# Kernel optimization log

Measured on AMD Instinct MI355X. Metric: run time of the kernel, lower is better.

The kernel has to match this reference:

```python
import jax, jax.numpy as jnp
import numpy as np

E_ROUTER = 32      # routed experts with real FFNs
ZERO_E = 8         # zero-experts (identity skip)
TOP_K = 4
ROUTED_SCALE = 2.5


def setup_inputs() -> dict:
    key = jax.random.key(0)
    k1, k2, k3, k4, k5 = jax.random.split(key, 5)
    T, H, I = 2048, 1024, 512
    N = E_ROUTER + ZERO_E
    return {
        "hidden_states": jax.random.normal(k1, (T, H), jnp.float32),
        "router_w": jax.random.normal(k2, (N, H), jnp.float32) * 0.02,            # classifier weight [N, H]
        "e_score_correction_bias": jax.random.normal(k3, (N,), jnp.float32) * 0.01,
        "w13": jax.random.normal(k4, (E_ROUTER, 2 * I, H), jnp.float32) * 0.02,   # gate+up per expert
        "w2": jax.random.normal(k5, (E_ROUTER, H, I), jnp.float32) * 0.02,        # down proj per expert
    }


def reference(hidden_states, router_w, e_score_correction_bias, w13, w2):
    T, H = hidden_states.shape
    I = w2.shape[-1]

    # --- router (LongcatFlashTopkRouter) ---
    logits = hidden_states @ router_w.T                         # [T, N]
    scores = jax.nn.softmax(logits, axis=-1)
    biased = scores + e_score_correction_bias[None, :]
    _, topk_ids = jax.lax.top_k(biased, TOP_K)                  # indices chosen on biased scores
    topk_w = jnp.take_along_axis(scores, topk_ids, axis=-1) * ROUTED_SCALE  # weights from unbiased scores

    # --- zero experts: ids >= E_ROUTER contribute weight * x directly ---
    zero_mask = topk_ids >= E_ROUTER
    zero_total = jnp.sum(jnp.where(zero_mask, topk_w, 0.0), axis=-1, keepdims=True)  # [T,1]
    zero_expert_output = hidden_states * zero_total
    topk_w = jnp.where(zero_mask, 0.0, topk_w)
    topk_ids = jnp.where(zero_mask, 0, topk_ids)

    # --- combine weights per (token, expert): scatter-add of topk weights ---
    combine = jnp.zeros((T, E_ROUTER), jnp.float32).at[
        jnp.arange(T)[:, None], topk_ids
    ].add(topk_w)                                               # [T, E]

    # --- experts: swiglu FFN per expert (dense form of grouped GEMM; zero combine
    #     weights make it mathematically identical to dispatch/compute/combine) ---
    gate_up = jnp.einsum('th,eih->eti', hidden_states, w13)     # [E, T, 2I]
    gate, up = gate_up[..., :I], gate_up[..., I:]
    h = jax.nn.silu(gate) * up                                  # [E, T, I]
    expert_out = jnp.einsum('eti,ehi->eth', h, w2)              # [E, T, H]
    routed = jnp.einsum('eth,te->th', expert_out, combine)      # [T, H]

    return routed + zero_expert_output
```

## Files before the change

kernel.cpp:

```cpp
#include <hip/hip_runtime.h>
#include <math.h>

#define TT 2048
#define HH 1024
#define NE 40
#define ER 32
#define II 512
#define TOPK 4
#define RSCALE 2.5f
#define MAXW 64

typedef __bf16 bf16x8 __attribute__((ext_vector_type(8)));
typedef float f32x4 __attribute__((ext_vector_type(4)));

__global__ __launch_bounds__(256) void k_router(const float* __restrict__ hidden,
                                                const float* __restrict__ rw,
                                                const float* __restrict__ bias,
                                                float* __restrict__ out,
                                                int* __restrict__ tok4_id,
                                                float* __restrict__ tok4_w,
                                                __bf16* __restrict__ hid_bf) {
  int lane = threadIdx.x & 63;
  int t = blockIdx.x * 4 + (threadIdx.x >> 6);
  const float* hrow = hidden + (size_t)t * HH;
  float4 hv[4];
  #pragma unroll
  for (int c = 0; c < 4; c++) hv[c] = *(const float4*)(hrow + c * 256 + lane * 4);

  float mylg = -INFINITY;
  for (int e = 0; e < NE; e++) {
    const float* wrow = rw + (size_t)e * HH;
    float p = 0.f;
    #pragma unroll
    for (int c = 0; c < 4; c++) {
      float4 w4 = *(const float4*)(wrow + c * 256 + lane * 4);
      p += hv[c].x * w4.x + hv[c].y * w4.y + hv[c].z * w4.z + hv[c].w * w4.w;
    }
    #pragma unroll
    for (int off = 32; off; off >>= 1) p += __shfl_xor(p, off);
    if (lane == e) mylg = p;
  }
  float m = mylg;
  #pragma unroll
  for (int off = 32; off; off >>= 1) m = fmaxf(m, __shfl_xor(m, off));
  float p = (lane < NE) ? expf(mylg - m) : 0.f;
  float s = p;
  #pragma unroll
  for (int off = 32; off; off >>= 1) s += __shfl_xor(s, off);
  float score = p / s;
  float v = (lane < NE) ? score + bias[lane] : -INFINITY;
  int ids[TOPK]; float wv[TOPK];
  #pragma unroll
  for (int k = 0; k < TOPK; k++) {
    float mv = v;
    int mi = (lane < NE) ? lane : 63;
    #pragma unroll
    for (int off = 32; off; off >>= 1) {
      float ov = __shfl_xor(mv, off);
      int oi = __shfl_xor(mi, off);
      if (ov > mv || (ov == mv && oi < mi)) { mv = ov; mi = oi; }
    }
    ids[k] = mi;
    wv[k] = RSCALE * __shfl(score, mi);
    if (lane == mi) v = -INFINITY;
  }
  float zt = 0.f;
  #pragma unroll
  for (int k = 0; k < TOPK; k++) if (ids[k] >= ER) zt += wv[k];
  if (lane == 0) {
    #pragma unroll
    for (int k = 0; k < TOPK; k++) {
      tok4_id[t * TOPK + k] = ids[k];
      tok4_w[t * TOPK + k] = wv[k];
    }
  }
  #pragma unroll
  for (int c = 0; c < 4; c++) {
    int j = c * 256 + lane * 4;
    float4 h4 = hv[c];
    *(float4*)(out + (size_t)t * HH + j) =
        make_float4(h4.x * zt, h4.y * zt, h4.z * zt, h4.w * zt);
    union { __bf16 h[4]; uint2 u; } pk;
    pk.h[0] = (__bf16)h4.x; pk.h[1] = (__bf16)h4.y;
    pk.h[2] = (__bf16)h4.z; pk.h[3] = (__bf16)h4.w;
    *(uint2*)(hid_bf + (size_t)t * HH + j) = pk.u;
  }
}

__global__ __launch_bounds__(256) void k_scanscatter(const int* __restrict__ tok4_id,
                                                     const float* __restrict__ tok4_w,
                                                     int* __restrict__ cnt,
                                                     int* __restrict__ offs,
                                                     int* __restrict__ wl_e,
                                                     int* __restrict__ wl_m0,
                                                     int* __restrict__ nwork,
                                                     int* __restrict__ pair_tok,
                                                     float* __restrict__ pair_w) {
  __shared__ int scnt[32];
  __shared__ int scur[32];
  int tid = threadIdx.x;
  if (tid < 32) scnt[tid] = 0;
  __syncthreads();
  int ids[32]; float wv[32];
  #pragma unroll
  for (int i = 0; i < 32; i++) {
    int idx = i * 256 + tid;
    ids[i] = tok4_id[idx];
    wv[i] = tok4_w[idx];
    if (ids[i] < ER) atomicAdd(&scnt[ids[i]], 1);
  }
  __syncthreads();
  if (tid < 64) {
    int lane = tid;
    int c = (lane < ER) ? scnt[lane] : 0;
    int ts = (c + 255) >> 8;
    int ps = c, pt = ts;
    #pragma unroll
    for (int off = 1; off < 32; off <<= 1) {
      int v1 = __shfl_up(ps, off);
      int v2 = __shfl_up(pt, off);
      if (lane >= off) { ps += v1; pt += v2; }
    }
    if (lane < ER) {
      int o = ps - c;
      offs[lane] = o; cnt[lane] = c; scur[lane] = o;
      int tb = pt - ts;
      for (int i = 0; i < ts; i++) { wl_e[tb + i] = lane; wl_m0[tb + i] = i * 256; }
    }
    if (lane == 31) *nwork = pt;
  }
  __syncthreads();
  #pragma unroll
  for (int i = 0; i < 32; i++) {
    if (ids[i] < ER) {
      int pos = atomicAdd(&scur[ids[i]], 1);
      pair_tok[pos] = (i * 256 + tid) >> 2;
      pair_w[pos] = wv[i];
    }
  }
}

__global__ __launch_bounds__(256) void k_w13(const __bf16* __restrict__ hid_bf,
                                             const float* __restrict__ w13,
                                             const int* __restrict__ cnt,
                                             const int* __restrict__ offs,
                                             const int* __restrict__ pair_tok,
                                             const int* __restrict__ wl_e,
                                             const int* __restrict__ wl_m0,
                                             const int* __restrict__ nwork,
                                             __bf16* __restrict__ h_buf) {
  int bx = blockIdx.x;
  if (bx >= *nwork) return;
  int e = wl_e[bx], m0w = wl_m0[bx];
  int M = cnt[e] - m0w; if (M > 256) M = 256;
  int base = offs[e] + m0w;
  int n0 = blockIdx.y * 32;

  __shared__ __bf16 As[256][72];
  __shared__ __bf16 Bs[64][72];
  __shared__ int tl[256];

  int tid = threadIdx.x;
  int lane = tid & 63, w = tid >> 6;
  int quad = lane >> 4, rr = lane & 15;

  tl[tid] = pair_tok[base + ((tid < M) ? tid : 0)];

  const float* wg_base = w13 + (size_t)e * (2 * II) * HH + (size_t)n0 * HH;
  const float* wu_base = w13 + (size_t)e * (2 * II) * HH + (size_t)(II + n0) * HH;

  f32x4 accg[4][2] = {};
  f32x4 accu[4][2] = {};
  __syncthreads();

  for (int k0 = 0; k0 < HH; k0 += 64) {
    #pragma unroll
    for (int p = 0; p < 8; p++) {
      int s = p * 256 + tid;
      int r = s >> 3, c = (s & 7) * 8;
      *(uint4*)&As[r][c] = *(const uint4*)(hid_bf + (size_t)tl[r] * HH + k0 + c);
    }
    #pragma unroll
    for (int p = 0; p < 4; p++) {
      int s = p * 256 + tid;
      int r = s >> 4, c = (s & 15) * 4;
      const float* src = ((r < 32) ? (wg_base + (size_t)r * HH)
                                   : (wu_base + (size_t)(r - 32) * HH)) + k0 + c;
      float4 v = *(const float4*)src;
      union { __bf16 h[4]; uint2 u; } pk;
      pk.h[0] = (__bf16)v.x; pk.h[1] = (__bf16)v.y;
      pk.h[2] = (__bf16)v.z; pk.h[3] = (__bf16)v.w;
      *(uint2*)&Bs[r][c] = pk.u;
    }
    __syncthreads();
    #pragma unroll
    for (int ks = 0; ks < 2; ks++) {
      int kb = ks * 32 + quad * 8;
      bf16x8 a[4], bg[2], bu[2];
      #pragma unroll
      for (int i = 0; i < 4; i++) a[i] = *(const bf16x8*)&As[w * 64 + i * 16 + rr][kb];
      #pragma unroll
      for (int j = 0; j < 2; j++) {
        bg[j] = *(const bf16x8*)&Bs[j * 16 + rr][kb];
        bu[j] = *(const bf16x8*)&Bs[32 + j * 16 + rr][kb];
      }
      #pragma unroll
      for (int i = 0; i < 4; i++)
        #pragma unroll
        for (int j = 0; j < 2; j++) {
          accg[i][j] = __builtin_amdgcn_mfma_f32_16x16x32_bf16(a[i], bg[j], accg[i][j], 0, 0, 0);
          accu[i][j] = __builtin_amdgcn_mfma_f32_16x16x32_bf16(a[i], bu[j], accu[i][j], 0, 0, 0);
        }
    }
    __syncthreads();
  }
  #pragma unroll
  for (int i = 0; i < 4; i++)
    #pragma unroll
    for (int j = 0; j < 2; j++)
      #pragma unroll
      for (int l = 0; l < 4; l++) {
        int m = w * 64 + i * 16 + quad * 4 + l;
        if (m < M) {
          float g = accg[i][j][l], u = accu[i][j][l];
          float hv = g / (1.f + expf(-g)) * u;
          h_buf[(size_t)(base + m) * II + n0 + j * 16 + rr] = (__bf16)hv;
        }
      }
}

__global__ __launch_bounds__(256) void k_w2(const __bf16* __restrict__ h_buf,
                                            const float* __restrict__ w2,
                                            const int* __restrict__ cnt,
                                            const int* __restrict__ offs,
                                            const int* __restrict__ pair_tok,
                                            const float* __restrict__ pair_w,
                                            const int* __restrict__ wl_e,
                                            const int* __restrict__ wl_m0,
                                            const int* __restrict__ nwork,
                                            float* __restrict__ out) {
  int bx = blockIdx.x;
  if (bx >= *nwork) return;
  int e = wl_e[bx], m0w = wl_m0[bx];
  int M = cnt[e] - m0w; if (M > 256) M = 256;
  int base = offs[e] + m0w;
  int h0 = blockIdx.y * 64;

  __shared__ __bf16 As[256][72];
  __shared__ __bf16 Bs[64][72];
  __shared__ int tl[256];
  __shared__ float wl[256];

  int tid = threadIdx.x;
  int lane = tid & 63, w = tid >> 6;
  int quad = lane >> 4, rr = lane & 15;

  {
    int ok = tid < M;
    tl[tid] = ok ? pair_tok[base + tid] : 0;
    wl[tid] = ok ? pair_w[base + tid] : 0.f;
  }
  const __bf16* h_base = h_buf + (size_t)base * II;
  const float* w_base = w2 + (size_t)e * HH * II + (size_t)h0 * II;

  f32x4 acc[4][4] = {};
  __syncthreads();

  for (int k0 = 0; k0 < II; k0 += 64) {
    #pragma unroll
    for (int p = 0; p < 8; p++) {
      int s = p * 256 + tid;
      int r = s >> 3, c = (s & 7) * 8;
      *(uint4*)&As[r][c] = *(const uint4*)(h_base + (size_t)r * II + k0 + c);
    }
    #pragma unroll
    for (int p = 0; p < 4; p++) {
      int s = p * 256 + tid;
      int r = s >> 4, c = (s & 15) * 4;
      float4 v = *(const float4*)(w_base + (size_t)r * II + k0 + c);
      union { __bf16 h[4]; uint2 u; } pk;
      pk.h[0] = (__bf16)v.x; pk.h[1] = (__bf16)v.y;
      pk.h[2] = (__bf16)v.z; pk.h[3] = (__bf16)v.w;
      *(uint2*)&Bs[r][c] = pk.u;
    }
    __syncthreads();
    #pragma unroll
    for (int ks = 0; ks < 2; ks++) {
      int kb = ks * 32 + quad * 8;
      bf16x8 a[4], b[4];
      #pragma unroll
      for (int i = 0; i < 4; i++) a[i] = *(const bf16x8*)&As[w * 64 + i * 16 + rr][kb];
      #pragma unroll
      for (int j = 0; j < 4; j++) b[j] = *(const bf16x8*)&Bs[j * 16 + rr][kb];
      #pragma unroll
      for (int i = 0; i < 4; i++)
        #pragma unroll
        for (int j = 0; j < 4; j++)
          acc[i][j] = __builtin_amdgcn_mfma_f32_16x16x32_bf16(a[i], b[j], acc[i][j], 0, 0, 0);
    }
    __syncthreads();
  }
  #pragma unroll
  for (int i = 0; i < 4; i++)
    #pragma unroll
    for (int l = 0; l < 4; l++) {
      int m = w * 64 + i * 16 + quad * 4 + l;
      if (m < M) {
        int t = tl[m];
        float wp = wl[m];
        #pragma unroll
        for (int j = 0; j < 4; j++)
          atomicAdd(&out[(size_t)t * HH + h0 + j * 16 + rr], acc[i][j][l] * wp);
      }
    }
}

extern "C" void kernel_launch(void* const* d_in, const int* in_sizes, int n_in,
                              void* d_out, int out_size, void* d_ws, size_t ws_size,
                              hipStream_t stream) {
  const float* hidden = (const float*)d_in[0];
  const float* rw     = (const float*)d_in[1];
  const float* bias   = (const float*)d_in[2];
  const float* w13    = (const float*)d_in[3];
  const float* w2     = (const float*)d_in[4];
  float* out = (float*)d_out;

  int* ws_i = (int*)d_ws;
  int* tok4_id = ws_i;
  float* tok4_w = (float*)(tok4_id + TT * TOPK);
  int* pair_tok = (int*)(tok4_w + TT * TOPK);
  float* pair_w = (float*)(pair_tok + TT * TOPK);
  int* cnt = (int*)(pair_w + TT * TOPK);
  int* offs = cnt + 32;
  int* wl_e = offs + 32;
  int* wl_m0 = wl_e + 64;
  int* nwork = wl_m0 + 64;
  __bf16* hid_bf = (__bf16*)(nwork + 64);
  __bf16* h_buf = hid_bf + (size_t)TT * HH;

  k_router<<<dim3(TT / 4), dim3(256), 0, stream>>>(hidden, rw, bias, out,
                                                   tok4_id, tok4_w, hid_bf);
  k_scanscatter<<<dim3(1), dim3(256), 0, stream>>>(tok4_id, tok4_w, cnt, offs,
                                                   wl_e, wl_m0, nwork, pair_tok, pair_w);
  k_w13<<<dim3(MAXW, 16), dim3(256), 0, stream>>>(hid_bf, w13, cnt, offs, pair_tok,
                                                  wl_e, wl_m0, nwork, h_buf);
  k_w2<<<dim3(MAXW, 16), dim3(256), 0, stream>>>(h_buf, w2, cnt, offs, pair_tok, pair_w,
                                                 wl_e, wl_m0, nwork, out);
}
```

Baseline: 340.8 us.

## Double-buffer expert GEMMs with async LDS loads, swizzle, and split scan/scatter

Rewrites the w13 and w2 expert GEMM kernels to double-buffer shared memory. Activation tiles are fetched with global_load_lds direct-to-LDS copies and weight tiles are prefetched into registers during the MFMA loop, using an XOR-swizzled unpadded LDS layout. N tiles are halved (16/32 columns) and the grid doubled for more blocks in flight. The single-block scan+scatter is split: expert counts are accumulated with atomics in the router, a tiny scan kernel builds offsets, and a 32-block scatter fills pairs. This adds a zero kernel and more launches, and makes pair ordering nondeterministic.

```diff
diff --git a/kernel.cpp b/kernel.cpp
--- a/kernel.cpp
+++ b/kernel.cpp
@@ -13,13 +13,31 @@
 typedef __bf16 bf16x8 __attribute__((ext_vector_type(8)));
 typedef float f32x4 __attribute__((ext_vector_type(4)));
 
+__device__ __forceinline__ void glds16(const void* g, void* l) {
+  __builtin_amdgcn_global_load_lds(
+      (const __attribute__((address_space(1))) unsigned int*)g,
+      (__attribute__((address_space(3))) unsigned int*)l, 16, 0, 0);
+}
+
+__device__ __forceinline__ void st_bf4(void* dst, float4 v) {
+  union { __bf16 h[4]; uint2 u; } pk;
+  pk.h[0] = (__bf16)v.x; pk.h[1] = (__bf16)v.y;
+  pk.h[2] = (__bf16)v.z; pk.h[3] = (__bf16)v.w;
+  *(uint2*)dst = pk.u;
+}
+
+__global__ __launch_bounds__(64) void k_zero(int* __restrict__ cnt) {
+  if (threadIdx.x < 32) cnt[threadIdx.x] = 0;
+}
+
 __global__ __launch_bounds__(256) void k_router(const float* __restrict__ hidden,
                                                 const float* __restrict__ rw,
                                                 const float* __restrict__ bias,
                                                 float* __restrict__ out,
                                                 int* __restrict__ tok4_id,
                                                 float* __restrict__ tok4_w,
-                                                __bf16* __restrict__ hid_bf) {
+                                                __bf16* __restrict__ hid_bf,
+                                                int* __restrict__ cnt) {
   int lane = threadIdx.x & 63;
   int t = blockIdx.x * 4 + (threadIdx.x >> 6);
   const float* hrow = hidden + (size_t)t * HH;
@@ -72,6 +90,7 @@
     for (int k = 0; k < TOPK; k++) {
       tok4_id[t * TOPK + k] = ids[k];
       tok4_w[t * TOPK + k] = wv[k];
+      if (ids[k] < ER) atomicAdd(&cnt[ids[k]], 1);
     }
   }
   #pragma unroll
@@ -87,56 +106,42 @@
   }
 }
 
-__global__ __launch_bounds__(256) void k_scanscatter(const int* __restrict__ tok4_id,
-                                                     const float* __restrict__ tok4_w,
-                                                     int* __restrict__ cnt,
-                                                     int* __restrict__ offs,
-                                                     int* __restrict__ wl_e,
-                                                     int* __restrict__ wl_m0,
-                                                     int* __restrict__ nwork,
-                                                     int* __restrict__ pair_tok,
-                                                     float* __restrict__ pair_w) {
-  __shared__ int scnt[32];
-  __shared__ int scur[32];
-  int tid = threadIdx.x;
-  if (tid < 32) scnt[tid] = 0;
-  __syncthreads();
-  int ids[32]; float wv[32];
-  #pragma unroll
-  for (int i = 0; i < 32; i++) {
-    int idx = i * 256 + tid;
-    ids[i] = tok4_id[idx];
-    wv[i] = tok4_w[idx];
-    if (ids[i] < ER) atomicAdd(&scnt[ids[i]], 1);
-  }
-  __syncthreads();
-  if (tid < 64) {
-    int lane = tid;
-    int c = (lane < ER) ? scnt[lane] : 0;
-    int ts = (c + 255) >> 8;
-    int ps = c, pt = ts;
-    #pragma unroll
-    for (int off = 1; off < 32; off <<= 1) {
-      int v1 = __shfl_up(ps, off);
-      int v2 = __shfl_up(pt, off);
-      if (lane >= off) { ps += v1; pt += v2; }
-    }
-    if (lane < ER) {
-      int o = ps - c;
-      offs[lane] = o; cnt[lane] = c; scur[lane] = o;
-      int tb = pt - ts;
-      for (int i = 0; i < ts; i++) { wl_e[tb + i] = lane; wl_m0[tb + i] = i * 256; }
-    }
-    if (lane == 31) *nwork = pt;
-  }
-  __syncthreads();
-  #pragma unroll
-  for (int i = 0; i < 32; i++) {
-    if (ids[i] < ER) {
-      int pos = atomicAdd(&scur[ids[i]], 1);
-      pair_tok[pos] = (i * 256 + tid) >> 2;
-      pair_w[pos] = wv[i];
-    }
+__global__ __launch_bounds__(64) void k_scan(const int* __restrict__ cnt,
+                                             int* __restrict__ offs,
+                                             int* __restrict__ wl_e,
+                                             int* __restrict__ wl_m0,
+                                             int* __restrict__ nwork,
+                                             int* __restrict__ gcur) {
+  int lane = threadIdx.x;
+  int c = (lane < ER) ? cnt[lane] : 0;
+  int ts = (c + 255) >> 8;
+  int ps = c, pt = ts;
+  #pragma unroll
+  for (int off = 1; off < 32; off <<= 1) {
+    int v1 = __shfl_up(ps, off);
+    int v2 = __shfl_up(pt, off);
+    if (lane >= off) { ps += v1; pt += v2; }
+  }
+  if (lane < ER) {
+    int o = ps - c;
+    offs[lane] = o; gcur[lane] = o;
+    int tb = pt - ts;
+    for (int i = 0; i < ts; i++) { wl_e[tb + i] = lane; wl_m0[tb + i] = i * 256; }
+  }
+  if (lane == 31) *nwork = pt;
+}
+
+__global__ __launch_bounds__(256) void k_scatter(const int* __restrict__ tok4_id,
+                                                 const float* __restrict__ tok4_w,
+                                                 int* __restrict__ gcur,
+                                                 int* __restrict__ pair_tok,
+                                                 float* __restrict__ pair_w) {
+  int idx = blockIdx.x * 256 + threadIdx.x;
+  int id = tok4_id[idx];
+  if (id < ER) {
+    int pos = atomicAdd(&gcur[id], 1);
+    pair_tok[pos] = idx >> 2;
+    pair_w[pos] = tok4_w[idx];
   }
 }
 
@@ -154,79 +159,93 @@
   int e = wl_e[bx], m0w = wl_m0[bx];
   int M = cnt[e] - m0w; if (M > 256) M = 256;
   int base = offs[e] + m0w;
-  int n0 = blockIdx.y * 32;
-
-  __shared__ __bf16 As[256][72];
-  __shared__ __bf16 Bs[64][72];
-  __shared__ int tl[256];
+  int n0 = blockIdx.y * 16;
+
+  __shared__ __bf16 As[2][256][64];
+  __shared__ __bf16 Bs[2][32][64];
 
   int tid = threadIdx.x;
   int lane = tid & 63, w = tid >> 6;
   int quad = lane >> 4, rr = lane & 15;
-
-  tl[tid] = pair_tok[base + ((tid < M) ? tid : 0)];
-
-  const float* wg_base = w13 + (size_t)e * (2 * II) * HH + (size_t)n0 * HH;
-  const float* wu_base = w13 + (size_t)e * (2 * II) * HH + (size_t)(II + n0) * HH;
-
-  f32x4 accg[4][2] = {};
-  f32x4 accu[4][2] = {};
+  int rx = rr & 7;
+  int lr = lane >> 3, lc = lane & 7;
+
+  const __bf16* asrc[8];
+  #pragma unroll
+  for (int p = 0; p < 8; p++) {
+    int row = p * 32 + w * 8 + lr;
+    int tok = pair_tok[base + ((row < M) ? row : 0)];
+    asrc[p] = hid_bf + (size_t)tok * HH + (lc ^ lr) * 8;
+  }
+  const float* wbase = w13 + (size_t)e * (2 * II) * HH;
+  const float* bsrc[2];
+  int boff[2];
+  #pragma unroll
+  for (int q = 0; q < 2; q++) {
+    int f = q * 256 + tid;
+    int row = f >> 4, c4 = f & 15;
+    int wrow = (row < 16) ? (n0 + row) : (II + n0 + row - 16);
+    bsrc[q] = wbase + (size_t)wrow * HH + c4 * 4;
+    boff[q] = row * 128 + (((c4 >> 1) ^ (row & 7)) << 4) + (c4 & 1) * 8;
+  }
+
+  #pragma unroll
+  for (int p = 0; p < 8; p++) glds16(asrc[p], &As[0][p * 32 + w * 8][0]);
+  #pragma unroll
+  for (int q = 0; q < 2; q++) st_bf4((char*)&Bs[0][0][0] + boff[q], *(const float4*)(bsrc[q]));
   __syncthreads();
 
-  for (int k0 = 0; k0 < HH; k0 += 64) {
-    #pragma unroll
-    for (int p = 0; p < 8; p++) {
-      int s = p * 256 + tid;
-      int r = s >> 3, c = (s & 7) * 8;
-      *(uint4*)&As[r][c] = *(const uint4*)(hid_bf + (size_t)tl[r] * HH + k0 + c);
-    }
-    #pragma unroll
-    for (int p = 0; p < 4; p++) {
-      int s = p * 256 + tid;
-      int r = s >> 4, c = (s & 15) * 4;
-      const float* src = ((r < 32) ? (wg_base + (size_t)r * HH)
-                                   : (wu_base + (size_t)(r - 32) * HH)) + k0 + c;
-      float4 v = *(const float4*)src;
-      union { __bf16 h[4]; uint2 u; } pk;
-      pk.h[0] = (__bf16)v.x; pk.h[1] = (__bf16)v.y;
-      pk.h[2] = (__bf16)v.z; pk.h[3] = (__bf16)v.w;
-      *(uint2*)&Bs[r][c] = pk.u;
+  f32x4 accg[4] = {};
+  f32x4 accu[4] = {};
+  int cur = 0;
+
+  for (int t = 0; t < HH / 64; t++) {
+    int nxt = cur ^ 1;
+    bool pf = (t + 1 < HH / 64);
+    float4 brA, brB;
+    if (pf) {
+      int k0n = (t + 1) * 64;
+      #pragma unroll
+      for (int p = 0; p < 8; p++) glds16(asrc[p] + k0n, &As[nxt][p * 32 + w * 8][0]);
+      brA = *(const float4*)(bsrc[0] + k0n);
+      brB = *(const float4*)(bsrc[1] + k0n);
+    }
+    const char* ac = (const char*)&As[cur][0][0];
+    const char* bc = (const char*)&Bs[cur][0][0];
+    #pragma unroll
+    for (int ks = 0; ks < 2; ks++) {
+      int cx = ((ks * 4 + quad) ^ rx) << 4;
+      bf16x8 av[4], bg, bu;
+      #pragma unroll
+      for (int i = 0; i < 4; i++)
+        av[i] = *(const bf16x8*)(ac + (w * 64 + i * 16 + rr) * 128 + cx);
+      bg = *(const bf16x8*)(bc + rr * 128 + cx);
+      bu = *(const bf16x8*)(bc + (16 + rr) * 128 + cx);
+      #pragma unroll
+      for (int i = 0; i < 4; i++) {
+        accg[i] = __builtin_amdgcn_mfma_f32_16x16x32_bf16(av[i], bg, accg[i], 0, 0, 0);
+        accu[i] = __builtin_amdgcn_mfma_f32_16x16x32_bf16(av[i], bu, accu[i], 0, 0, 0);
+      }
+    }
+    if (pf) {
+      st_bf4((char*)&Bs[nxt][0][0] + boff[0], brA);
+      st_bf4((char*)&Bs[nxt][0][0] + boff[1], brB);
     }
     __syncthreads();
-    #pragma unroll
-    for (int ks = 0; ks < 2; ks++) {
-      int kb = ks * 32 + quad * 8;
-      bf16x8 a[4], bg[2], bu[2];
-      #pragma unroll
-      for (int i = 0; i < 4; i++) a[i] = *(const bf16x8*)&As[w * 64 + i * 16 + rr][kb];
-      #pragma unroll
-      for (int j = 0; j < 2; j++) {
-        bg[j] = *(const bf16x8*)&Bs[j * 16 + rr][kb];
-        bu[j] = *(const bf16x8*)&Bs[32 + j * 16 + rr][kb];
+    cur ^= 1;
+  }
+
+  #pragma unroll
+  for (int i = 0; i < 4; i++)
+    #pragma unroll
+    for (int l = 0; l < 4; l++) {
+      int m = w * 64 + i * 16 + quad * 4 + l;
+      if (m < M) {
+        float g = accg[i][l], u = accu[i][l];
+        float hv = g / (1.f + expf(-g)) * u;
+        h_buf[(size_t)(base + m) * II + n0 + rr] = (__bf16)hv;
       }
-      #pragma unroll
-      for (int i = 0; i < 4; i++)
-        #pragma unroll
-        for (int j = 0; j < 2; j++) {
-          accg[i][j] = __builtin_amdgcn_mfma_f32_16x16x32_bf16(a[i], bg[j], accg[i][j], 0, 0, 0);
-          accu[i][j] = __builtin_amdgcn_mfma_f32_16x16x32_bf16(a[i], bu[j], accu[i][j], 0, 0, 0);
-        }
-    }
-    __syncthreads();
-  }
-  #pragma unroll
-  for (int i = 0; i < 4; i++)
-    #pragma unroll
-    for (int j = 0; j < 2; j++)
-      #pragma unroll
-      for (int l = 0; l < 4; l++) {
-        int m = w * 64 + i * 16 + quad * 4 + l;
-        if (m < M) {
-          float g = accg[i][j][l], u = accu[i][j][l];
-          float hv = g / (1.f + expf(-g)) * u;
-          h_buf[(size_t)(base + m) * II + n0 + j * 16 + rr] = (__bf16)hv;
-        }
-      }
+    }
 }
 
 __global__ __launch_bounds__(256) void k_w2(const __bf16* __restrict__ h_buf,
@@ -244,62 +263,88 @@
   int e = wl_e[bx], m0w = wl_m0[bx];
   int M = cnt[e] - m0w; if (M > 256) M = 256;
   int base = offs[e] + m0w;
-  int h0 = blockIdx.y * 64;
-
-  __shared__ __bf16 As[256][72];
-  __shared__ __bf16 Bs[64][72];
+  int h0 = blockIdx.y * 32;
+
+  __shared__ __bf16 As[2][256][64];
+  __shared__ __bf16 Bs[2][32][64];
   __shared__ int tl[256];
   __shared__ float wl[256];
 
   int tid = threadIdx.x;
   int lane = tid & 63, w = tid >> 6;
   int quad = lane >> 4, rr = lane & 15;
+  int rx = rr & 7;
+  int lr = lane >> 3, lc = lane & 7;
 
   {
     int ok = tid < M;
     tl[tid] = ok ? pair_tok[base + tid] : 0;
     wl[tid] = ok ? pair_w[base + tid] : 0.f;
   }
-  const __bf16* h_base = h_buf + (size_t)base * II;
-  const float* w_base = w2 + (size_t)e * HH * II + (size_t)h0 * II;
-
-  f32x4 acc[4][4] = {};
+
+  const __bf16* asrc[8];
+  #pragma unroll
+  for (int p = 0; p < 8; p++) {
+    int row = p * 32 + w * 8 + lr;
+    asrc[p] = h_buf + (size_t)(base + row) * II + (lc ^ lr) * 8;
+  }
+  const float* w_base = w2 + (size_t)e * HH * II;
+  const float* bsrc[2];
+  int boff[2];
+  #pragma unroll
+  for (int q = 0; q < 2; q++) {
+    int f = q * 256 + tid;
+    int row = f >> 4, c4 = f & 15;
+    bsrc[q] = w_base + (size_t)(h0 + row) * II + c4 * 4;
+    boff[q] = row * 128 + (((c4 >> 1) ^ (row & 7)) << 4) + (c4 & 1) * 8;
+  }
+
+  #pragma unroll
+  for (int p = 0; p < 8; p++) glds16(asrc[p], &As[0][p * 32 + w * 8][0]);
+  #pragma unroll
+  for (int q = 0; q < 2; q++) st_bf4((char*)&Bs[0][0][0] + boff[q], *(const float4*)(bsrc[q]));
   __syncthreads();
 
-  for (int k0 = 0; k0 < II; k0 += 64) {
-    #pragma unroll
-    for (int p = 0; p < 8; p++) {
-      int s = p * 256 + tid;
-      int r = s >> 3, c = (s & 7) * 8;
-      *(uint4*)&As[r][c] = *(const uint4*)(h_base + (size_t)r * II + k0 + c);
-    }
-    #pragma unroll
-    for (int p = 0; p < 4; p++) {
-      int s = p * 256 + tid;
-      int r = s >> 4, c = (s & 15) * 4;
-      float4 v = *(const float4*)(w_base + (size_t)r * II + k0 + c);
-      union { __bf16 h[4]; uint2 u; } pk;
-      pk.h[0] = (__bf16)v.x; pk.h[1] = (__bf16)v.y;
-      pk.h[2] = (__bf16)v.z; pk.h[3] = (__bf16)v.w;
-      *(uint2*)&Bs[r][c] = pk.u;
-    }
-    __syncthreads();
+  f32x4 acc[4][2] = {};
+  int cur = 0;
+
+  for (int t = 0; t < II / 64; t++) {
+    int nxt = cur ^ 1;
+    bool pf = (t + 1 < II / 64);
+    float4 brA, brB;
+    if (pf) {
+      int k0n = (t + 1) * 64;
+      #pragma unroll
+      for (int p = 0; p < 8; p++) glds16(asrc[p] + k0n, &As[nxt][p * 32 + w * 8][0]);
+      brA = *(const float4*)(bsrc[0] + k0n);
+      brB = *(const float4*)(bsrc[1] + k0n);
+    }
+    const char* ac = (const char*)&As[cur][0][0];
+    const char* bc = (const char*)&Bs[cur][0][0];
     #pragma unroll
     for (int ks = 0; ks < 2; ks++) {
-      int kb = ks * 32 + quad * 8;
-      bf16x8 a[4], b[4];
-      #pragma unroll
-      for (int i = 0; i < 4; i++) a[i] = *(const bf16x8*)&As[w * 64 + i * 16 + rr][kb];
-      #pragma unroll
-      for (int j = 0; j < 4; j++) b[j] = *(const bf16x8*)&Bs[j * 16 + rr][kb];
+      int cx = ((ks * 4 + quad) ^ rx) << 4;
+      bf16x8 av[4], b[2];
+      #pragma unroll
+      for (int i = 0; i < 4; i++)
+        av[i] = *(const bf16x8*)(ac + (w * 64 + i * 16 + rr) * 128 + cx);
+      #pragma unroll
+      for (int j = 0; j < 2; j++)
+        b[j] = *(const bf16x8*)(bc + (j * 16 + rr) * 128 + cx);
       #pragma unroll
       for (int i = 0; i < 4; i++)
         #pragma unroll
-        for (int j = 0; j < 4; j++)
-          acc[i][j] = __builtin_amdgcn_mfma_f32_16x16x32_bf16(a[i], b[j], acc[i][j], 0, 0, 0);
+        for (int j = 0; j < 2; j++)
+          acc[i][j] = __builtin_amdgcn_mfma_f32_16x16x32_bf16(av[i], b[j], acc[i][j], 0, 0, 0);
+    }
+    if (pf) {
+      st_bf4((char*)&Bs[nxt][0][0] + boff[0], brA);
+      st_bf4((char*)&Bs[nxt][0][0] + boff[1], brB);
     }
     __syncthreads();
-  }
+    cur ^= 1;
+  }
+
   #pragma unroll
   for (int i = 0; i < 4; i++)
     #pragma unroll
@@ -309,7 +354,7 @@
         int t = tl[m];
         float wp = wl[m];
         #pragma unroll
-        for (int j = 0; j < 4; j++)
+        for (int j = 0; j < 2; j++)
           atomicAdd(&out[(size_t)t * HH + h0 + j * 16 + rr], acc[i][j][l] * wp);
       }
     }
@@ -335,15 +380,17 @@
   int* wl_e = offs + 32;
   int* wl_m0 = wl_e + 64;
   int* nwork = wl_m0 + 64;
+  int* gcur = nwork + 16;
   __bf16* hid_bf = (__bf16*)(nwork + 64);
   __bf16* h_buf = hid_bf + (size_t)TT * HH;
 
+  k_zero<<<dim3(1), dim3(64), 0, stream>>>(cnt);
   k_router<<<dim3(TT / 4), dim3(256), 0, stream>>>(hidden, rw, bias, out,
-                                                   tok4_id, tok4_w, hid_bf);
-  k_scanscatter<<<dim3(1), dim3(256), 0, stream>>>(tok4_id, tok4_w, cnt, offs,
-                                                   wl_e, wl_m0, nwork, pair_tok, pair_w);
-  k_w13<<<dim3(MAXW, 16), dim3(256), 0, stream>>>(hid_bf, w13, cnt, offs, pair_tok,
+                                                   tok4_id, tok4_w, hid_bf, cnt);
+  k_scan<<<dim3(1), dim3(64), 0, stream>>>(cnt, offs, wl_e, wl_m0, nwork, gcur);
+  k_scatter<<<dim3(32), dim3(256), 0, stream>>>(tok4_id, tok4_w, gcur, pair_tok, pair_w);
+  k_w13<<<dim3(MAXW, 32), dim3(256), 0, stream>>>(hid_bf, w13, cnt, offs, pair_tok,
                                                   wl_e, wl_m0, nwork, h_buf);
-  k_w2<<<dim3(MAXW, 16), dim3(256), 0, stream>>>(h_buf, w2, cnt, offs, pair_tok, pair_w,
+  k_w2<<<dim3(MAXW, 32), dim3(256), 0, stream>>>(h_buf, w2, cnt, offs, pair_tok, pair_w,
                                                  wl_e, wl_m0, nwork, out);
 }
```

Result: slower. 444.2 us (+30.4%).
